# Optimization experiments

Measured on AMD Instinct MI355X. Metric: run time of the kernel, lower is better.

The kernel has to match this reference:

```python
import math
import jax, jax.numpy as jnp
import numpy as np

SQRT_2_OVER_PI = 0.7978845608028654
FACIL_RATE = 2.0
FIRE_THRESH = 0.88
EPS = 1e-05

def _gelu(x):
    return 0.5 * x * (1.0 + jnp.tanh(SQRT_2_OVER_PI * (x + 0.044715 * x ** 3)))

def setup_inputs() -> dict:
    key = jax.random.key(0)
    ks = jax.random.split(key, 8)
    B, T, D, N = 4, 4096, 1024, 512
    x = jax.random.normal(ks[0], (B, T, D), jnp.float32)
    ema_x = jax.random.normal(ks[1], (D,), jnp.float32) * 0.1
    ema_x2 = ema_x ** 2 + jax.random.uniform(ks[2], (D,), jnp.float32) + 0.5
    ema_y = jax.random.normal(ks[3], (D,), jnp.float32) * 0.1
    ema_y2 = ema_y ** 2 + jax.random.uniform(ks[4], (D,), jnp.float32) + 0.5
    buf = jax.random.normal(ks[5], (N, D), jnp.float32)
    buf = buf / jnp.linalg.norm(buf, axis=-1, keepdims=True)
    facil = 1.0 + 2.0 * jax.random.uniform(ks[6], (N,), jnp.float32)  # facilitation levels >= 1
    mask = jnp.ones((N,), dtype=bool)
    return {
        'x': x,
        'log_tau_in': jnp.float32(math.log(1.0)),
        'log_tau_out': jnp.float32(math.log(1.0)),
        'log_a_in': jnp.float32(0.0),
        'log_a_out': jnp.float32(0.0),
        'log_k_boost': jnp.float32(math.log(0.5)),
        'log_k_damp': jnp.float32(math.log(0.3)),
        'ema_x': ema_x, 'ema_x2': ema_x2, 'ema_y': ema_y, 'ema_y2': ema_y2,
        'buf': buf, 'facil': facil, 'mask': mask,
    }

def reference(x, log_tau_in, log_tau_out, log_a_in, log_a_out,
              log_k_boost, log_k_damp, ema_x, ema_x2, ema_y, ema_y2,
              buf, facil, mask):
    sg = jax.lax.stop_gradient
    D = x.shape[-1]
    y = _gelu(x)
    # --- gate_211 (l1_ready steady state); z-statistics are detached in torch ---
    tau_in, tau_out = jnp.exp(log_tau_in), jnp.exp(log_tau_out)
    a_in, a_out = jax.nn.sigmoid(log_a_in), jax.nn.sigmoid(log_a_out)
    std_x = jnp.sqrt(jnp.clip(sg(ema_x2) - sg(ema_x) ** 2, 0.0)) + EPS
    z_in = jnp.mean(((sg(x) - sg(ema_x)) / std_x) ** 2, axis=-1)        # [B,T]
    std_y = jnp.sqrt(jnp.clip(sg(ema_y2) - sg(ema_y) ** 2, 0.0)) + EPS
    z_out = jnp.mean(((sg(y) - sg(ema_y)) / std_y) ** 2, axis=-1)       # [B,T]
    g_in = 1.0 - a_in + a_in * jnp.exp(-tau_in * z_in)
    g_out = 1.0 - a_out + a_out * jnp.exp(-tau_out * z_out)
    gate = g_in * g_out
    y1 = y * gate[..., None]
    # --- eval-time OCS nearest-neighbor facilitation (l2_ready, pass1_complete) ---
    k_boost = jnp.clip(jnp.exp(log_k_boost), 0.01, 4.0)
    k_damp = jnp.clip(jnp.exp(log_k_damp), 0.01, 0.9)
    y1_mean = jnp.mean(sg(y1).reshape(-1, D), axis=0)                    # [D]
    m_n = y1_mean / jnp.maximum(jnp.linalg.norm(y1_mean), 1e-12)
    buf_sg = sg(buf)
    buf_n = buf_sg / jnp.maximum(jnp.linalg.norm(buf_sg, axis=-1, keepdims=True), 1e-12)
    sims = jnp.where(mask, buf_n @ m_n, -1.0)                            # [N]
    nearest_idx = jnp.argmax(sims)
    sim_val = jnp.clip(sims[nearest_idx], 0.0, 1.0)
    fired = sim_val > FIRE_THRESH
    facil_level = sg(facil)[nearest_idx] * jnp.where(fired, FACIL_RATE, 1.0)
    v = buf_sg[nearest_idx]                                              # [D]
    valid = jnp.all(jnp.isfinite(v)) & (jnp.linalg.norm(v) >= 1e-06)
    mod = (facil_level - 1.0) * sim_val
    boost = 1.0 + sg(k_boost) * mod            # torch uses .item(): detached
    damp = jnp.maximum(0.01, 1.0 - sg(k_damp) * mod)
    proj = jnp.sum(y1 * v, axis=-1, keepdims=True)
    y_par = proj * v
    out = jnp.where(valid, y_par * boost + (y1 - y_par) * damp, y1)
    return out
```

## Files before the change

### kernel.cpp

```cpp
#include <hip/hip_runtime.h>
#include <math.h>

#define D 1024
#define NROWS 16384
#define NBUF 512

#define OFF_MEAN 0
#define OFF_KEY  1024
#define OFF_GATE 2048
#define OFF_PART 20480
#define ZERO_BYTES 4112

typedef float nfloat4 __attribute__((ext_vector_type(4)));

__device__ __forceinline__ float4 ld4(const float* p) { return *(const float4*)p; }
__device__ __forceinline__ void st4_nt(float* p, float4 v) {
    nfloat4 nv = { v.x, v.y, v.z, v.w };
    __builtin_nontemporal_store(nv, (nfloat4*)p);
}

__device__ __forceinline__ float wave_red(float v) {
    #pragma unroll
    for (int off = 32; off > 0; off >>= 1) v += __shfl_xor(v, off, 64);
    return v;
}

__device__ __forceinline__ float gelu_f(float x) {
    float u = 0.7978845608028654f * (x + 0.044715f * x * x * x);
    float e = __expf(2.0f * u);
    float t = 1.0f - 2.0f / (e + 1.0f);
    return 0.5f * x * (1.0f + t);
}

__device__ __forceinline__ float4 inv_std4(float4 m, float4 m2) {
    float4 r;
    r.x = 1.0f / (sqrtf(fmaxf(m2.x - m.x * m.x, 0.f)) + 1e-5f);
    r.y = 1.0f / (sqrtf(fmaxf(m2.y - m.y * m.y, 0.f)) + 1e-5f);
    r.z = 1.0f / (sqrtf(fmaxf(m2.z - m.z * m.z, 0.f)) + 1e-5f);
    r.w = 1.0f / (sqrtf(fmaxf(m2.w - m.w * m.w, 0.f)) + 1e-5f);
    return r;
}

template<int RPW>
__global__ __launch_bounds__(256, 4) void k_passA(const float* __restrict__ x,
                                                  const float* __restrict__ ema_x,
                                                  const float* __restrict__ ema_x2,
                                                  const float* __restrict__ ema_y,
                                                  const float* __restrict__ ema_y2,
                                                  const float* __restrict__ lti,
                                                  const float* __restrict__ lto,
                                                  const float* __restrict__ lai,
                                                  const float* __restrict__ lao,
                                                  float* __restrict__ ws) {
    __shared__ float s_acc[D];
    const int tid = threadIdx.x;
    const int wave = tid >> 6, lane = tid & 63;
    for (int i = tid; i < D; i += 256) s_acc[i] = 0.0f;
    __syncthreads();

    const float tau_in = __expf(lti[0]), tau_out = __expf(lto[0]);
    const float a_in  = 1.0f / (1.0f + __expf(-lai[0]));
    const float a_out = 1.0f / (1.0f + __expf(-lao[0]));

    int col[4];
    float4 emx[4], isx[4], emy[4], isy[4];
    #pragma unroll
    for (int j = 0; j < 4; ++j) {
        col[j] = 4 * lane + 256 * j;
        emx[j] = ld4(&ema_x[col[j]]);
        isx[j] = inv_std4(emx[j], ld4(&ema_x2[col[j]]));
        emy[j] = ld4(&ema_y[col[j]]);
        isy[j] = inv_std4(emy[j], ld4(&ema_y2[col[j]]));
    }
    float4 acc[4];
    #pragma unroll
    for (int j = 0; j < 4; ++j) acc[j] = make_float4(0.f, 0.f, 0.f, 0.f);

    const int r0 = (blockIdx.x * 4 + wave) * RPW;
    for (int r = r0; r < r0 + RPW; ++r) {
        const float* xr = x + (size_t)r * D;
        float4 yv[4];
        float zin = 0.f, zout = 0.f;
        #pragma unroll
        for (int j = 0; j < 4; ++j) {
            float4 xv = ld4(&xr[col[j]]);
            float dx, dy;
            dx = (xv.x - emx[j].x) * isx[j].x; zin += dx * dx;
            dx = (xv.y - emx[j].y) * isx[j].y; zin += dx * dx;
            dx = (xv.z - emx[j].z) * isx[j].z; zin += dx * dx;
            dx = (xv.w - emx[j].w) * isx[j].w; zin += dx * dx;
            yv[j].x = gelu_f(xv.x); dy = (yv[j].x - emy[j].x) * isy[j].x; zout += dy * dy;
            yv[j].y = gelu_f(xv.y); dy = (yv[j].y - emy[j].y) * isy[j].y; zout += dy * dy;
            yv[j].z = gelu_f(xv.z); dy = (yv[j].z - emy[j].z) * isy[j].z; zout += dy * dy;
            yv[j].w = gelu_f(xv.w); dy = (yv[j].w - emy[j].w) * isy[j].w; zout += dy * dy;
        }
        zin  = wave_red(zin)  * (1.0f / D);
        zout = wave_red(zout) * (1.0f / D);
        float g = ((1.0f - a_in)  + a_in  * __expf(-tau_in  * zin)) *
                  ((1.0f - a_out) + a_out * __expf(-tau_out * zout));
        if (lane == 0) ws[OFF_GATE + r] = g;
        #pragma unroll
        for (int j = 0; j < 4; ++j) {
            acc[j].x += yv[j].x * g;
            acc[j].y += yv[j].y * g;
            acc[j].z += yv[j].z * g;
            acc[j].w += yv[j].w * g;
        }
    }
    #pragma unroll
    for (int j = 0; j < 4; ++j) {
        atomicAdd(&s_acc[col[j] + 0], acc[j].x);
        atomicAdd(&s_acc[col[j] + 1], acc[j].y);
        atomicAdd(&s_acc[col[j] + 2], acc[j].z);
        atomicAdd(&s_acc[col[j] + 3], acc[j].w);
    }
    __syncthreads();
    float4 pv = *(float4*)&s_acc[tid * 4];
    *(float4*)&ws[OFF_PART + (size_t)blockIdx.x * D + tid * 4] = pv;
}

__global__ __launch_bounds__(256) void k_mean(float* __restrict__ ws) {
    const int tid = threadIdx.x;
    const float* P = &ws[OFF_PART + (size_t)blockIdx.x * 16 * D];
    float4 s = make_float4(0.f, 0.f, 0.f, 0.f);
    #pragma unroll
    for (int i = 0; i < 16; ++i) {
        float4 v = ld4(&P[(size_t)i * D + 4 * tid]);
        s.x += v.x; s.y += v.y; s.z += v.z; s.w += v.w;
    }
    atomicAdd(&ws[OFF_MEAN + 4 * tid + 0], s.x);
    atomicAdd(&ws[OFF_MEAN + 4 * tid + 1], s.y);
    atomicAdd(&ws[OFF_MEAN + 4 * tid + 2], s.z);
    atomicAdd(&ws[OFF_MEAN + 4 * tid + 3], s.w);
}

__global__ __launch_bounds__(256) void k_sims(const float* __restrict__ buf,
                                              const unsigned char* __restrict__ mask,
                                              float* __restrict__ ws) {
    __shared__ float s_red[4];
    __shared__ float s_inv;
    const int tid = threadIdx.x, wave = tid >> 6, lane = tid & 63;

    float4 mv = ld4(&ws[OFF_MEAN + tid * 4]);
    float ns = mv.x * mv.x + mv.y * mv.y + mv.z * mv.z + mv.w * mv.w;
    ns = wave_red(ns);
    if (lane == 0) s_red[wave] = ns;
    __syncthreads();
    if (tid == 0) {
        float t = s_red[0] + s_red[1] + s_red[2] + s_red[3];
        s_inv = 1.0f / fmaxf(sqrtf(t), 1e-12f);
    }
    __syncthreads();
    const float inv = s_inv;

    int col[4];
    float4 mvv[4];
    #pragma unroll
    for (int j = 0; j < 4; ++j) {
        col[j] = 4 * lane + 256 * j;
        mvv[j] = ld4(&ws[OFF_MEAN + col[j]]);
    }
    const int n = blockIdx.x * 4 + wave;
    const float* br = buf + (size_t)n * D;
    float dot = 0.f, bns = 0.f;
    #pragma unroll
    for (int j = 0; j < 4; ++j) {
        float4 bv = ld4(&br[col[j]]);
        dot += bv.x * mvv[j].x + bv.y * mvv[j].y + bv.z * mvv[j].z + bv.w * mvv[j].w;
        bns += bv.x * bv.x + bv.y * bv.y + bv.z * bv.z + bv.w * bv.w;
    }
    dot = wave_red(dot);
    bns = wave_red(bns);
    if (lane == 0) {
        float sim = -1.0f;
        if (mask[n]) sim = (dot * inv) / fmaxf(sqrtf(bns), 1e-12f);
        unsigned int fb = __float_as_uint(sim);
        unsigned int mono = (fb & 0x80000000u) ? ~fb : (fb | 0x80000000u);
        unsigned long long key = ((unsigned long long)mono << 32) | (unsigned int)(~n);
        atomicMax((unsigned long long*)&ws[OFF_KEY], key);
    }
}

__global__ __launch_bounds__(256, 4) void k_passB(const float* __restrict__ x,
                                                  const float* __restrict__ buf,
                                                  const float* __restrict__ facil,
                                                  const float* __restrict__ lkb,
                                                  const float* __restrict__ lkd,
                                                  const float* __restrict__ ws,
                                                  float* __restrict__ out) {
    __shared__ float s_red[4];
    __shared__ float s_sc[3];
    const int tid = threadIdx.x, wave = tid >> 6, lane = tid & 63;

    const unsigned long long key = *(const unsigned long long*)&ws[OFF_KEY];
    const int idx = (int)(~(unsigned int)(key & 0xFFFFFFFFull));
    const unsigned int mono = (unsigned int)(key >> 32);
    const unsigned int fb = (mono & 0x80000000u) ? (mono ^ 0x80000000u) : ~mono;
    const float sim = __uint_as_float(fb);

    int col[4];
    float4 vv[4];
    const float* vrow = buf + (size_t)idx * D;
    float bns = 0.f;
    #pragma unroll
    for (int j = 0; j < 4; ++j) {
        col[j] = 4 * lane + 256 * j;
        vv[j] = ld4(&vrow[col[j]]);
        if (!isfinite(vv[j].x)) bns = __uint_as_float(0x7FC00000u);
        if (!isfinite(vv[j].y)) bns = __uint_as_float(0x7FC00000u);
        if (!isfinite(vv[j].z)) bns = __uint_as_float(0x7FC00000u);
        if (!isfinite(vv[j].w)) bns = __uint_as_float(0x7FC00000u);
        bns += vv[j].x * vv[j].x + vv[j].y * vv[j].y + vv[j].z * vv[j].z + vv[j].w * vv[j].w;
    }
    bns = wave_red(bns);
    if (lane == 0) s_red[wave] = bns;
    __syncthreads();
    if (tid == 0) {
        float t = s_red[0] + s_red[1] + s_red[2] + s_red[3];
        int valid = (t >= 1e-12f) ? 1 : 0;
        float sim_val = fminf(fmaxf(sim, 0.0f), 1.0f);
        float fl = facil[idx] * ((sim_val > 0.88f) ? 2.0f : 1.0f);
        float mod = (fl - 1.0f) * sim_val;
        float kb = fminf(fmaxf(__expf(lkb[0]), 0.01f), 4.0f);
        float kd = fminf(fmaxf(__expf(lkd[0]), 0.01f), 0.9f);
        float boost = 1.0f + kb * mod;
        float damp = fmaxf(0.01f, 1.0f - kd * mod);
        s_sc[0] = valid ? damp : 1.0f;
        s_sc[1] = valid ? (boost - damp) : 0.0f;
        s_sc[2] = (float)valid;
    }
    __syncthreads();
    const float dampe = s_sc[0], coef = s_sc[1];
    if (s_sc[2] == 0.0f) {
        #pragma unroll
        for (int j = 0; j < 4; ++j) vv[j] = make_float4(0.f, 0.f, 0.f, 0.f);
    }

    const int r0 = (blockIdx.x * 4 + wave) * 2;
    for (int r = r0; r < r0 + 2; ++r) {
        const float* xr = x + (size_t)r * D;
        const float g = ws[OFF_GATE + r];
        float4 y1[4];
        float proj = 0.f;
        #pragma unroll
        for (int j = 0; j < 4; ++j) {
            float4 xv = ld4(&xr[col[j]]);
            y1[j].x = gelu_f(xv.x) * g; proj += y1[j].x * vv[j].x;
            y1[j].y = gelu_f(xv.y) * g; proj += y1[j].y * vv[j].y;
            y1[j].z = gelu_f(xv.z) * g; proj += y1[j].z * vv[j].z;
            y1[j].w = gelu_f(xv.w) * g; proj += y1[j].w * vv[j].w;
        }
        proj = wave_red(proj);
        const float pc = proj * coef;
        float* orow = out + (size_t)r * D;
        #pragma unroll
        for (int j = 0; j < 4; ++j) {
            float4 o;
            o.x = y1[j].x * dampe + pc * vv[j].x;
            o.y = y1[j].y * dampe + pc * vv[j].y;
            o.z = y1[j].z * dampe + pc * vv[j].z;
            o.w = y1[j].w * dampe + pc * vv[j].w;
            st4_nt(&orow[col[j]], o);
        }
    }
}

extern "C" void kernel_launch(void* const* d_in, const int* in_sizes, int n_in,
                              void* d_out, int out_size, void* d_ws, size_t ws_size,
                              hipStream_t stream) {
    const float* x      = (const float*)d_in[0];
    const float* lti    = (const float*)d_in[1];
    const float* lto    = (const float*)d_in[2];
    const float* lai    = (const float*)d_in[3];
    const float* lao    = (const float*)d_in[4];
    const float* lkb    = (const float*)d_in[5];
    const float* lkd    = (const float*)d_in[6];
    const float* ema_x  = (const float*)d_in[7];
    const float* ema_x2 = (const float*)d_in[8];
    const float* ema_y  = (const float*)d_in[9];
    const float* ema_y2 = (const float*)d_in[10];
    const float* buf    = (const float*)d_in[11];
    const float* facil  = (const float*)d_in[12];
    const unsigned char* mask = (const unsigned char*)d_in[13];
    float* ws  = (float*)d_ws;
    float* out = (float*)d_out;

    int NP;
    if      (ws_size >= ((size_t)OFF_PART + 2048u * D) * 4) NP = 2048;
    else if (ws_size >= ((size_t)OFF_PART + 1024u * D) * 4) NP = 1024;
    else                                                    NP = 512;

    (void)hipMemsetAsync(d_ws, 0, ZERO_BYTES, stream);
    if (NP == 2048)
        hipLaunchKernelGGL(k_passA<2>, dim3(2048), dim3(256), 0, stream,
                           x, ema_x, ema_x2, ema_y, ema_y2, lti, lto, lai, lao, ws);
    else if (NP == 1024)
        hipLaunchKernelGGL(k_passA<4>, dim3(1024), dim3(256), 0, stream,
                           x, ema_x, ema_x2, ema_y, ema_y2, lti, lto, lai, lao, ws);
    else
        hipLaunchKernelGGL(k_passA<8>, dim3(512), dim3(256), 0, stream,
                           x, ema_x, ema_x2, ema_y, ema_y2, lti, lto, lai, lao, ws);
    hipLaunchKernelGGL(k_mean,  dim3(NP / 16), dim3(256), 0, stream, ws);
    hipLaunchKernelGGL(k_sims,  dim3(128), dim3(256), 0, stream, buf, mask, ws);
    hipLaunchKernelGGL(k_passB, dim3(2048), dim3(256), 0, stream,
                       x, buf, facil, lkb, lkd, ws, out);
}
```

Measured before the change: 217.8 us.

## Precompute EMA statistics in init kernel, stage in LDS, simplify GELU math

Replaces the memset with a small init kernel that precomputes per-column scale/offset (a, a*mean) for the z-statistics and the scalar gate constants, and zeroes the accumulators. Pass A loads these into shared memory instead of recomputing inverse std per block, and uses FMA forms. GELU is rewritten as x - x/(1+exp(2u)) with a hardware reciprocal. Pass B stages the buffer vector in shared memory and switches nontemporal stores to regular stores. These changes reduce register pressure and ALU work in an otherwise memory-bound pipeline, at the cost of extra LDS traffic and one more launch, and regular stores may pollute cache.

```diff
diff --git a/kernel.cpp b/kernel.cpp
--- a/kernel.cpp
+++ b/kernel.cpp
@@ -5,19 +5,20 @@
 #define NROWS 16384
 #define NBUF 512
 
-#define OFF_MEAN 0
-#define OFF_KEY  1024
-#define OFF_GATE 2048
-#define OFF_PART 20480
-#define ZERO_BYTES 4112
+#define OFF_STAT 0
+#define OFF_AX   0
+#define OFF_BX   1024
+#define OFF_AY   2048
+#define OFF_BY   3072
+#define OFF_MEAN 4096
+#define OFF_KEY  5120
+#define OFF_CONST 5124
+#define OFF_GATE 5632
+#define OFF_PART 22016
 
 typedef float nfloat4 __attribute__((ext_vector_type(4)));
 
 __device__ __forceinline__ float4 ld4(const float* p) { return *(const float4*)p; }
-__device__ __forceinline__ void st4_nt(float* p, float4 v) {
-    nfloat4 nv = { v.x, v.y, v.z, v.w };
-    __builtin_nontemporal_store(nv, (nfloat4*)p);
-}
 
 __device__ __forceinline__ float wave_red(float v) {
     #pragma unroll
@@ -26,52 +27,69 @@
 }
 
 __device__ __forceinline__ float gelu_f(float x) {
-    float u = 0.7978845608028654f * (x + 0.044715f * x * x * x);
-    float e = __expf(2.0f * u);
-    float t = 1.0f - 2.0f / (e + 1.0f);
-    return 0.5f * x * (1.0f + t);
-}
-
-__device__ __forceinline__ float4 inv_std4(float4 m, float4 m2) {
-    float4 r;
-    r.x = 1.0f / (sqrtf(fmaxf(m2.x - m.x * m.x, 0.f)) + 1e-5f);
-    r.y = 1.0f / (sqrtf(fmaxf(m2.y - m.y * m.y, 0.f)) + 1e-5f);
-    r.z = 1.0f / (sqrtf(fmaxf(m2.z - m.z * m.z, 0.f)) + 1e-5f);
-    r.w = 1.0f / (sqrtf(fmaxf(m2.w - m.w * m.w, 0.f)) + 1e-5f);
-    return r;
+    float x2 = x * x;
+    float t1 = fmaf(0.044715f, x2, 1.0f);
+    float u2 = (1.5957691216057308f * x) * t1;
+    float e  = __expf(u2);
+    float r  = __builtin_amdgcn_rcpf(e + 1.0f);
+    return fmaf(-x, r, x);
+}
+
+__device__ __forceinline__ float4 gelu4(float4 x) {
+    float4 y;
+    y.x = gelu_f(x.x); y.y = gelu_f(x.y); y.z = gelu_f(x.z); y.w = gelu_f(x.w);
+    return y;
+}
+
+__global__ void k_init(const float* __restrict__ ema_x, const float* __restrict__ ema_x2,
+                       const float* __restrict__ ema_y, const float* __restrict__ ema_y2,
+                       const float* __restrict__ lti, const float* __restrict__ lto,
+                       const float* __restrict__ lai, const float* __restrict__ lao,
+                       float* __restrict__ ws) {
+    int t = threadIdx.x;
+    if (t < D) {
+        float mx = ema_x[t];
+        float vx = fmaxf(ema_x2[t] - mx * mx, 0.0f);
+        float ax = 1.0f / (sqrtf(vx) + 1e-5f);
+        ws[OFF_AX + t] = ax;
+        ws[OFF_BX + t] = mx * ax;
+        float my = ema_y[t];
+        float vy = fmaxf(ema_y2[t] - my * my, 0.0f);
+        float ay = 1.0f / (sqrtf(vy) + 1e-5f);
+        ws[OFF_AY + t] = ay;
+        ws[OFF_BY + t] = my * ay;
+        ws[OFF_MEAN + t] = 0.0f;
+    }
+    if (t == 0) {
+        *(unsigned long long*)&ws[OFF_KEY] = 0ull;
+        ws[OFF_CONST + 0] = __expf(lti[0]);
+        ws[OFF_CONST + 1] = __expf(lto[0]);
+        ws[OFF_CONST + 2] = 1.0f / (1.0f + __expf(-lai[0]));
+        ws[OFF_CONST + 3] = 1.0f / (1.0f + __expf(-lao[0]));
+    }
 }
 
 template<int RPW>
 __global__ __launch_bounds__(256, 4) void k_passA(const float* __restrict__ x,
-                                                  const float* __restrict__ ema_x,
-                                                  const float* __restrict__ ema_x2,
-                                                  const float* __restrict__ ema_y,
-                                                  const float* __restrict__ ema_y2,
-                                                  const float* __restrict__ lti,
-                                                  const float* __restrict__ lto,
-                                                  const float* __restrict__ lai,
-                                                  const float* __restrict__ lao,
                                                   float* __restrict__ ws) {
+    __shared__ float s_stat[4096];
     __shared__ float s_acc[D];
     const int tid = threadIdx.x;
     const int wave = tid >> 6, lane = tid & 63;
-    for (int i = tid; i < D; i += 256) s_acc[i] = 0.0f;
-    __syncthreads();
-
-    const float tau_in = __expf(lti[0]), tau_out = __expf(lto[0]);
-    const float a_in  = 1.0f / (1.0f + __expf(-lai[0]));
-    const float a_out = 1.0f / (1.0f + __expf(-lao[0]));
+
+    for (int i = tid; i < 1024; i += 256) {
+        *(float4*)&s_stat[4 * i] = ld4(&ws[OFF_STAT + 4 * i]);
+        s_acc[i] = 0.0f;
+    }
+    __syncthreads();
+
+    const float tau_in = ws[OFF_CONST + 0], tau_out = ws[OFF_CONST + 1];
+    const float a_in  = ws[OFF_CONST + 2], a_out  = ws[OFF_CONST + 3];
 
     int col[4];
-    float4 emx[4], isx[4], emy[4], isy[4];
-    #pragma unroll
-    for (int j = 0; j < 4; ++j) {
-        col[j] = 4 * lane + 256 * j;
-        emx[j] = ld4(&ema_x[col[j]]);
-        isx[j] = inv_std4(emx[j], ld4(&ema_x2[col[j]]));
-        emy[j] = ld4(&ema_y[col[j]]);
-        isy[j] = inv_std4(emy[j], ld4(&ema_y2[col[j]]));
-    }
+    #pragma unroll
+    for (int j = 0; j < 4; ++j) col[j] = 4 * lane + 256 * j;
+
     float4 acc[4];
     #pragma unroll
     for (int j = 0; j < 4; ++j) acc[j] = make_float4(0.f, 0.f, 0.f, 0.f);
@@ -79,20 +97,29 @@
     const int r0 = (blockIdx.x * 4 + wave) * RPW;
     for (int r = r0; r < r0 + RPW; ++r) {
         const float* xr = x + (size_t)r * D;
+        float4 xv[4];
+        #pragma unroll
+        for (int j = 0; j < 4; ++j) xv[j] = ld4(&xr[col[j]]);
+
         float4 yv[4];
         float zin = 0.f, zout = 0.f;
         #pragma unroll
         for (int j = 0; j < 4; ++j) {
-            float4 xv = ld4(&xr[col[j]]);
-            float dx, dy;
-            dx = (xv.x - emx[j].x) * isx[j].x; zin += dx * dx;
-            dx = (xv.y - emx[j].y) * isx[j].y; zin += dx * dx;
-            dx = (xv.z - emx[j].z) * isx[j].z; zin += dx * dx;
-            dx = (xv.w - emx[j].w) * isx[j].w; zin += dx * dx;
-            yv[j].x = gelu_f(xv.x); dy = (yv[j].x - emy[j].x) * isy[j].x; zout += dy * dy;
-            yv[j].y = gelu_f(xv.y); dy = (yv[j].y - emy[j].y) * isy[j].y; zout += dy * dy;
-            yv[j].z = gelu_f(xv.z); dy = (yv[j].z - emy[j].z) * isy[j].z; zout += dy * dy;
-            yv[j].w = gelu_f(xv.w); dy = (yv[j].w - emy[j].w) * isy[j].w; zout += dy * dy;
+            float4 a = *(const float4*)&s_stat[OFF_AX + col[j]];
+            float4 b = *(const float4*)&s_stat[OFF_BX + col[j]];
+            float dx;
+            dx = fmaf(xv[j].x, a.x, -b.x); zin = fmaf(dx, dx, zin);
+            dx = fmaf(xv[j].y, a.y, -b.y); zin = fmaf(dx, dx, zin);
+            dx = fmaf(xv[j].z, a.z, -b.z); zin = fmaf(dx, dx, zin);
+            dx = fmaf(xv[j].w, a.w, -b.w); zin = fmaf(dx, dx, zin);
+            yv[j] = gelu4(xv[j]);
+            float4 ay = *(const float4*)&s_stat[OFF_AY + col[j]];
+            float4 by = *(const float4*)&s_stat[OFF_BY + col[j]];
+            float dy;
+            dy = fmaf(yv[j].x, ay.x, -by.x); zout = fmaf(dy, dy, zout);
+            dy = fmaf(yv[j].y, ay.y, -by.y); zout = fmaf(dy, dy, zout);
+            dy = fmaf(yv[j].z, ay.z, -by.z); zout = fmaf(dy, dy, zout);
+            dy = fmaf(yv[j].w, ay.w, -by.w); zout = fmaf(dy, dy, zout);
         }
         zin  = wave_red(zin)  * (1.0f / D);
         zout = wave_red(zout) * (1.0f / D);
@@ -101,10 +128,10 @@
         if (lane == 0) ws[OFF_GATE + r] = g;
         #pragma unroll
         for (int j = 0; j < 4; ++j) {
-            acc[j].x += yv[j].x * g;
-            acc[j].y += yv[j].y * g;
-            acc[j].z += yv[j].z * g;
-            acc[j].w += yv[j].w * g;
+            acc[j].x = fmaf(yv[j].x, g, acc[j].x);
+            acc[j].y = fmaf(yv[j].y, g, acc[j].y);
+            acc[j].z = fmaf(yv[j].z, g, acc[j].z);
+            acc[j].w = fmaf(yv[j].w, g, acc[j].w);
         }
     }
     #pragma unroll
@@ -115,8 +142,7 @@
         atomicAdd(&s_acc[col[j] + 3], acc[j].w);
     }
     __syncthreads();
-    float4 pv = *(float4*)&s_acc[tid * 4];
-    *(float4*)&ws[OFF_PART + (size_t)blockIdx.x * D + tid * 4] = pv;
+    *(float4*)&ws[OFF_PART + (size_t)blockIdx.x * D + 4 * tid] = *(float4*)&s_acc[4 * tid];
 }
 
 __global__ __launch_bounds__(256) void k_mean(float* __restrict__ ws) {
@@ -188,6 +214,7 @@
                                                   const float* __restrict__ lkd,
                                                   const float* __restrict__ ws,
                                                   float* __restrict__ out) {
+    __shared__ float s_v[D];
     __shared__ float s_red[4];
     __shared__ float s_sc[3];
     const int tid = threadIdx.x, wave = tid >> 6, lane = tid & 63;
@@ -198,20 +225,11 @@
     const unsigned int fb = (mono & 0x80000000u) ? (mono ^ 0x80000000u) : ~mono;
     const float sim = __uint_as_float(fb);
 
-    int col[4];
-    float4 vv[4];
-    const float* vrow = buf + (size_t)idx * D;
+    float4 vt = ld4(&buf[(size_t)idx * D + 4 * tid]);
     float bns = 0.f;
-    #pragma unroll
-    for (int j = 0; j < 4; ++j) {
-        col[j] = 4 * lane + 256 * j;
-        vv[j] = ld4(&vrow[col[j]]);
-        if (!isfinite(vv[j].x)) bns = __uint_as_float(0x7FC00000u);
-        if (!isfinite(vv[j].y)) bns = __uint_as_float(0x7FC00000u);
-        if (!isfinite(vv[j].z)) bns = __uint_as_float(0x7FC00000u);
-        if (!isfinite(vv[j].w)) bns = __uint_as_float(0x7FC00000u);
-        bns += vv[j].x * vv[j].x + vv[j].y * vv[j].y + vv[j].z * vv[j].z + vv[j].w * vv[j].w;
-    }
+    if (!isfinite(vt.x) || !isfinite(vt.y) || !isfinite(vt.z) || !isfinite(vt.w))
+        bns = __uint_as_float(0x7FC00000u);
+    bns += vt.x * vt.x + vt.y * vt.y + vt.z * vt.z + vt.w * vt.w;
     bns = wave_red(bns);
     if (lane == 0) s_red[wave] = bns;
     __syncthreads();
@@ -231,24 +249,30 @@
     }
     __syncthreads();
     const float dampe = s_sc[0], coef = s_sc[1];
-    if (s_sc[2] == 0.0f) {
-        #pragma unroll
-        for (int j = 0; j < 4; ++j) vv[j] = make_float4(0.f, 0.f, 0.f, 0.f);
-    }
+    if (s_sc[2] == 0.0f) vt = make_float4(0.f, 0.f, 0.f, 0.f);
+    *(float4*)&s_v[4 * tid] = vt;
+    __syncthreads();
+
+    int col[4];
+    #pragma unroll
+    for (int j = 0; j < 4; ++j) col[j] = 4 * lane + 256 * j;
 
     const int r0 = (blockIdx.x * 4 + wave) * 2;
     for (int r = r0; r < r0 + 2; ++r) {
         const float* xr = x + (size_t)r * D;
         const float g = ws[OFF_GATE + r];
-        float4 y1[4];
+        float4 y1[4], vv[4];
         float proj = 0.f;
         #pragma unroll
         for (int j = 0; j < 4; ++j) {
             float4 xv = ld4(&xr[col[j]]);
-            y1[j].x = gelu_f(xv.x) * g; proj += y1[j].x * vv[j].x;
-            y1[j].y = gelu_f(xv.y) * g; proj += y1[j].y * vv[j].y;
-            y1[j].z = gelu_f(xv.z) * g; proj += y1[j].z * vv[j].z;
-            y1[j].w = gelu_f(xv.w) * g; proj += y1[j].w * vv[j].w;
+            vv[j] = *(const float4*)&s_v[col[j]];
+            y1[j] = gelu4(xv);
+            y1[j].x *= g; y1[j].y *= g; y1[j].z *= g; y1[j].w *= g;
+            proj = fmaf(y1[j].x, vv[j].x, proj);
+            proj = fmaf(y1[j].y, vv[j].y, proj);
+            proj = fmaf(y1[j].z, vv[j].z, proj);
+            proj = fmaf(y1[j].w, vv[j].w, proj);
         }
         proj = wave_red(proj);
         const float pc = proj * coef;
@@ -256,11 +280,11 @@
         #pragma unroll
         for (int j = 0; j < 4; ++j) {
             float4 o;
-            o.x = y1[j].x * dampe + pc * vv[j].x;
-            o.y = y1[j].y * dampe + pc * vv[j].y;
-            o.z = y1[j].z * dampe + pc * vv[j].z;
-            o.w = y1[j].w * dampe + pc * vv[j].w;
-            st4_nt(&orow[col[j]], o);
+            o.x = fmaf(y1[j].x, dampe, pc * vv[j].x);
+            o.y = fmaf(y1[j].y, dampe, pc * vv[j].y);
+            o.z = fmaf(y1[j].z, dampe, pc * vv[j].z);
+            o.w = fmaf(y1[j].w, dampe, pc * vv[j].w);
+            *(float4*)&orow[col[j]] = o;
         }
     }
 }
@@ -290,18 +314,16 @@
     else if (ws_size >= ((size_t)OFF_PART + 1024u * D) * 4) NP = 1024;
     else                                                    NP = 512;
 
-    (void)hipMemsetAsync(d_ws, 0, ZERO_BYTES, stream);
+    hipLaunchKernelGGL(k_init, dim3(1), dim3(1024), 0, stream,
+                       ema_x, ema_x2, ema_y, ema_y2, lti, lto, lai, lao, ws);
     if (NP == 2048)
-        hipLaunchKernelGGL(k_passA<2>, dim3(2048), dim3(256), 0, stream,
-                           x, ema_x, ema_x2, ema_y, ema_y2, lti, lto, lai, lao, ws);
+        hipLaunchKernelGGL(k_passA<2>, dim3(2048), dim3(256), 0, stream, x, ws);
     else if (NP == 1024)
-        hipLaunchKernelGGL(k_passA<4>, dim3(1024), dim3(256), 0, stream,
-                           x, ema_x, ema_x2, ema_y, ema_y2, lti, lto, lai, lao, ws);
+        hipLaunchKernelGGL(k_passA<4>, dim3(1024), dim3(256), 0, stream, x, ws);
     else
-        hipLaunchKernelGGL(k_passA<8>, dim3(512), dim3(256), 0, stream,
-                           x, ema_x, ema_x2, ema_y, ema_y2, lti, lto, lai, lao, ws);
-    hipLaunchKernelGGL(k_mean,  dim3(NP / 16), dim3(256), 0, stream, ws);
-    hipLaunchKernelGGL(k_sims,  dim3(128), dim3(256), 0, stream, buf, mask, ws);
+        hipLaunchKernelGGL(k_passA<8>, dim3(512), dim3(256), 0, stream, x, ws);
+    hipLaunchKernelGGL(k_mean, dim3(NP / 16), dim3(256), 0, stream, ws);
+    hipLaunchKernelGGL(k_sims, dim3(128), dim3(256), 0, stream, buf, mask, ws);
     hipLaunchKernelGGL(k_passB, dim3(2048), dim3(256), 0, stream,
                        x, buf, facil, lkb, lkd, ws, out);
 }
```

Result: no change. 214.3 us (-1.6%).
